# Performance work log

Measured on AMD Instinct MI355X. Metric: run time of the kernel, lower is better.

The kernel has to match this reference:

```python
import jax, jax.numpy as jnp
import numpy as np

H = 2048      # num_hidden
B = 2048      # batch_size
T = 64        # seq_length
C = 10        # num_classes


def setup_inputs() -> dict:
    key = jax.random.key(0)
    k = jax.random.split(key, 4)
    bound = float(np.sqrt(1.0 / H))  # uniform(-bound, bound) init as in the torch module
    return {
        "x": jax.random.normal(k[0], (B, T), dtype=jnp.float32),
        "W_hx": jax.random.uniform(k[1], (H, 1), jnp.float32, -bound, bound),
        "W_hh": jax.random.uniform(k[2], (H, H), jnp.float32, -bound, bound),
        "W_hy": jax.random.uniform(k[3], (H, C), jnp.float32, -bound, bound),
        "b_h": jnp.zeros((H, 1), jnp.float32),
        "b_p": jnp.zeros((C, 1), jnp.float32),
    }


def reference(x, W_hx, W_hh, W_hy, b_h, b_p):
    # x: [B, T]; hidden state kept as [H, B] to match the torch layout.
    xT = x.T  # [T, B] so scan iterates over time

    def step(h, xt):
        # W_hx @ x_t  : [H,1] @ [1,B] -> [H,B]; W_hh @ h : [H,B]
        h = jnp.tanh(W_hx @ xt[None, :] + W_hh @ h + b_h)
        return h, None

    h0 = jnp.zeros((W_hh.shape[0], x.shape[0]), x.dtype)
    hT, _ = jax.lax.scan(step, h0, xT)
    out = W_hy.T @ hT + b_p  # [C, B]
    return out.T             # [B, C]
```

## Files before the change

kernel.cpp:

```cpp
#include <hip/hip_runtime.h>
#include <cstdint>
#include <cstddef>
#include <cmath>

#define H  2048
#define BB 2048
#define TT 64
#define NC 10
#define BK 64

typedef __bf16 bf16;
typedef bf16  bf16x8 __attribute__((ext_vector_type(8)));
typedef bf16  bf16x4 __attribute__((ext_vector_type(4)));
typedef float f32x4  __attribute__((ext_vector_type(4)));

__device__ __forceinline__ void load_lds16(const void* g, void* l) {
    __builtin_amdgcn_global_load_lds(
        (__attribute__((address_space(1))) void*)(void*)g,
        (__attribute__((address_space(3))) void*)l,
        16, 0, 0);
}

__global__ void w_shuffle_kernel(const float* __restrict__ Whh,
                                 bf16* __restrict__ Wshuf) {
    int tid = blockIdx.x * blockDim.x + threadIdx.x;
    int sub = tid >> 6;
    int l   = tid & 63;
    int n16 = sub >> 6;
    int k32 = sub & 63;
    int n = n16 * 16 + (l & 15);
    int k = k32 * 32 + (l >> 4) * 8;
    const float* src = Whh + (size_t)n * H + k;
    bf16x8 o;
#pragma unroll
    for (int j = 0; j < 8; ++j) o[j] = (bf16)src[j];
    *(bf16x8*)(Wshuf + (size_t)tid * 8) = o;
}

__global__ void rnn_init(const float* __restrict__ x,
                         const float* __restrict__ Whx,
                         const float* __restrict__ bh,
                         bf16* __restrict__ S) {
    int b  = blockIdx.x;
    int i0 = threadIdx.x * 8;
    float xv = x[(size_t)b * TT];
    bf16x8 o;
#pragma unroll
    for (int j = 0; j < 8; ++j)
        o[j] = (bf16)tanhf(Whx[i0 + j] * xv + bh[i0 + j]);
    *(bf16x8*)(S + (size_t)b * H + i0) = o;
}

__launch_bounds__(256)
__global__ void rnn_step(const float* __restrict__ x,
                         const float* __restrict__ Whx,
                         const float* __restrict__ bh,
                         const bf16*  __restrict__ Wshuf,
                         const bf16*  __restrict__ Sr,
                         bf16* __restrict__ Sw,
                         int t) {
    __shared__ __align__(16) bf16 As[2][128 * BK];

    const int tid  = threadIdx.x;
    const int w    = tid >> 6;
    const int lane = tid & 63;

    const int xcd = blockIdx.x & 7;
    const int loc = blockIdx.x >> 3;
    const int bm0 = (xcd * 2 + (loc & 1)) * 128;
    const int bn0 = (loc >> 1) * 64;

    const int qm   = (w & 1) * 64;
    const int qn   = (w >> 1) * 32;
    const int lrow = lane & 15;
    const int quad = lane >> 4;

    const int s_r = tid >> 3;
    const int s_l = tid & 7;

    const int nb16 = (bn0 + qn) >> 4;
    const bf16* wb = Wshuf + (size_t)lane * 8;

    auto stageA = [&](int b, int k0) {
#pragma unroll
        for (int i = 0; i < 4; ++i) {
            int r = i * 32 + s_r;
            int g = s_l ^ (r & 7);
            load_lds16(Sr + (size_t)(bm0 + r) * H + k0 + g * 8,
                       &As[b][(i * 256 + w * 64) * 8]);
        }
    };
    auto loadB = [&](bf16x8 (&B)[2][2], int k0) {
        const int kb32 = k0 >> 5;
#pragma unroll
        for (int kc = 0; kc < 2; ++kc)
#pragma unroll
            for (int fn = 0; fn < 2; ++fn)
                B[kc][fn] = *(const bf16x8*)(wb +
                    ((size_t)(nb16 + fn) * 64 + kb32 + kc) * 512);
    };

    f32x4 acc[4][2];
#pragma unroll
    for (int i = 0; i < 4; ++i)
#pragma unroll
        for (int j = 0; j < 2; ++j) acc[i][j] = (f32x4){0.f, 0.f, 0.f, 0.f};

    auto compute = [&](const bf16* Ab, bf16x8 (&B)[2][2]) {
#pragma unroll
        for (int kc = 0; kc < 2; ++kc) {
            bf16x8 af[4];
#pragma unroll
            for (int f = 0; f < 4; ++f) {
                int row = qm + f * 16 + lrow;
                int g   = kc * 4 + quad;
                int l   = g ^ (row & 7);
                af[f] = *(const bf16x8*)&Ab[(row * 8 + l) * 8];
            }
#pragma unroll
            for (int fm = 0; fm < 4; ++fm)
#pragma unroll
                for (int fn = 0; fn < 2; ++fn)
                    acc[fm][fn] = __builtin_amdgcn_mfma_f32_16x16x32_bf16(
                        af[fm], B[kc][fn], acc[fm][fn], 0, 0, 0);
        }
    };

    bf16x8 B0[2][2], B1[2][2];
    stageA(0, 0);
    loadB(B0, 0);

    for (int k0 = 0; k0 < H; k0 += 2 * BK) {
        __syncthreads();
        if (k0 + BK < H) { loadB(B1, k0 + BK); stageA(1, k0 + BK); }
        compute(As[0], B0);

        __syncthreads();
        if (k0 + 2 * BK < H) { loadB(B0, k0 + 2 * BK); stageA(0, k0 + 2 * BK); }
        compute(As[1], B1);
    }

#pragma unroll
    for (int fm = 0; fm < 4; ++fm) {
        int rb = bm0 + qm + fm * 16 + quad * 4;
        float xv[4];
#pragma unroll
        for (int r = 0; r < 4; ++r) xv[r] = x[(size_t)(rb + r) * TT + t];
#pragma unroll
        for (int fn = 0; fn < 2; ++fn) {
            int col = bn0 + qn + fn * 16 + lrow;
            float wx = Whx[col], bb = bh[col];
#pragma unroll
            for (int r = 0; r < 4; ++r) {
                float z = acc[fm][fn][r] + wx * xv[r] + bb;
                Sw[(size_t)(rb + r) * H + col] = (bf16)tanhf(z);
            }
        }
    }
}

__global__ void out_proj(const bf16* __restrict__ S,
                         const float* __restrict__ Why,
                         const float* __restrict__ bp,
                         float* __restrict__ out) {
    int b = blockIdx.x, tid = threadIdx.x;
    float p[NC];
#pragma unroll
    for (int c = 0; c < NC; ++c) p[c] = 0.f;
    for (int h = tid; h < H; h += 256) {
        float s = (float)S[(size_t)b * H + h];
        const float* wr = Why + h * NC;
#pragma unroll
        for (int c = 0; c < NC; ++c) p[c] += s * wr[c];
    }
    __shared__ float red[256 * NC];
#pragma unroll
    for (int c = 0; c < NC; ++c) red[tid * NC + c] = p[c];
    __syncthreads();
    for (int s = 128; s > 0; s >>= 1) {
        if (tid < s)
#pragma unroll
            for (int c = 0; c < NC; ++c) red[tid * NC + c] += red[(tid + s) * NC + c];
        __syncthreads();
    }
    if (tid < NC) out[(size_t)b * NC + tid] = red[tid] + bp[tid];
}

extern "C" void kernel_launch(void* const* d_in, const int* in_sizes, int n_in,
                              void* d_out, int out_size, void* d_ws, size_t ws_size,
                              hipStream_t stream) {
    const float* x   = (const float*)d_in[0];
    const float* Whx = (const float*)d_in[1];
    const float* Whh = (const float*)d_in[2];
    const float* Why = (const float*)d_in[3];
    const float* bh  = (const float*)d_in[4];
    const float* bp  = (const float*)d_in[5];
    float* out = (float*)d_out;

    bf16* Wshuf = (bf16*)d_ws;
    bf16* S0 = (bf16*)((char*)d_ws + (size_t)8 * 1024 * 1024);
    bf16* S1 = (bf16*)((char*)d_ws + (size_t)16 * 1024 * 1024);

    hipLaunchKernelGGL(w_shuffle_kernel, dim3((H * H / 8) / 256), dim3(256),
                       0, stream, Whh, Wshuf);

    hipLaunchKernelGGL(rnn_init, dim3(BB), dim3(256), 0, stream, x, Whx, bh, S1);

    for (int t = 1; t < TT; ++t) {
        const bf16* Srd = (t & 1) ? S1 : S0;
        bf16*       Swr = (t & 1) ? S0 : S1;
        hipLaunchKernelGGL(rnn_step, dim3(512), dim3(256), 0, stream,
                           x, Whx, bh, Wshuf, Srd, Swr, t);
    }

    hipLaunchKernelGGL(out_proj, dim3(BB), dim3(256), 0, stream, S0, Why, bp, out);
}
```

Before: 1.782 ms.

## Drop LDS staging and load A fragments directly from global in 512-thread blocks

The per-step GEMM kernel stops staging the hidden-state tile through shared memory. Each wave now reads its A and B MFMA fragments straight from global memory into registers, double-buffered in registers, with bare s_barrier calls used to keep the waves in step. Blocks grow to 512 threads covering a 128x128 output tile with 256 blocks, so there are fewer, larger blocks. This removes LDS traffic and __syncthreads overhead, but A fragments are no longer shared across waves, so global and L2 traffic goes up and load-latency hiding depends on the register double buffer.

New measurement: 4.792 ms. 169% more time.

```diff
diff --git a/kernel.cpp b/kernel.cpp
--- a/kernel.cpp
+++ b/kernel.cpp
@@ -7,19 +7,10 @@
 #define BB 2048
 #define TT 64
 #define NC 10
-#define BK 64
 
 typedef __bf16 bf16;
 typedef bf16  bf16x8 __attribute__((ext_vector_type(8)));
-typedef bf16  bf16x4 __attribute__((ext_vector_type(4)));
 typedef float f32x4  __attribute__((ext_vector_type(4)));
-
-__device__ __forceinline__ void load_lds16(const void* g, void* l) {
-    __builtin_amdgcn_global_load_lds(
-        (__attribute__((address_space(1))) void*)(void*)g,
-        (__attribute__((address_space(3))) void*)l,
-        16, 0, 0);
-}
 
 __global__ void w_shuffle_kernel(const float* __restrict__ Whh,
                                  bf16* __restrict__ Wshuf) {
@@ -51,7 +42,7 @@
     *(bf16x8*)(S + (size_t)b * H + i0) = o;
 }
 
-__launch_bounds__(256)
+__launch_bounds__(512, 2)
 __global__ void rnn_step(const float* __restrict__ x,
                          const float* __restrict__ Whx,
                          const float* __restrict__ bh,
@@ -59,46 +50,30 @@
                          const bf16*  __restrict__ Sr,
                          bf16* __restrict__ Sw,
                          int t) {
-    __shared__ __align__(16) bf16 As[2][128 * BK];
-
     const int tid  = threadIdx.x;
     const int w    = tid >> 6;
     const int lane = tid & 63;
+    const int lrow = lane & 15;
+    const int quad = lane >> 4;
 
     const int xcd = blockIdx.x & 7;
     const int loc = blockIdx.x >> 3;
     const int bm0 = (xcd * 2 + (loc & 1)) * 128;
-    const int bn0 = (loc >> 1) * 64;
+    const int bn0 = (loc >> 1) * 128;
 
-    const int qm   = (w & 1) * 64;
-    const int qn   = (w >> 1) * 32;
-    const int lrow = lane & 15;
-    const int quad = lane >> 4;
+    const int ms = w & 1;
+    const int ns = w >> 1;
 
-    const int s_r = tid >> 3;
-    const int s_l = tid & 7;
+    const bf16* pA[4];
+#pragma unroll
+    for (int fm = 0; fm < 4; ++fm)
+        pA[fm] = Sr + (size_t)(bm0 + ms * 64 + fm * 16 + lrow) * H + quad * 8;
 
-    const int nb16 = (bn0 + qn) >> 4;
-    const bf16* wb = Wshuf + (size_t)lane * 8;
-
-    auto stageA = [&](int b, int k0) {
+    const bf16* pB[2];
 #pragma unroll
-        for (int i = 0; i < 4; ++i) {
-            int r = i * 32 + s_r;
-            int g = s_l ^ (r & 7);
-            load_lds16(Sr + (size_t)(bm0 + r) * H + k0 + g * 8,
-                       &As[b][(i * 256 + w * 64) * 8]);
-        }
-    };
-    auto loadB = [&](bf16x8 (&B)[2][2], int k0) {
-        const int kb32 = k0 >> 5;
-#pragma unroll
-        for (int kc = 0; kc < 2; ++kc)
-#pragma unroll
-            for (int fn = 0; fn < 2; ++fn)
-                B[kc][fn] = *(const bf16x8*)(wb +
-                    ((size_t)(nb16 + fn) * 64 + kb32 + kc) * 512);
-    };
+    for (int fn = 0; fn < 2; ++fn)
+        pB[fn] = Wshuf + ((size_t)(((bn0 + ns * 32) >> 4) + fn) * 64) * 512
+                       + (size_t)lane * 8;
 
     f32x4 acc[4][2];
 #pragma unroll
@@ -106,49 +81,54 @@
 #pragma unroll
         for (int j = 0; j < 2; ++j) acc[i][j] = (f32x4){0.f, 0.f, 0.f, 0.f};
 
-    auto compute = [&](const bf16* Ab, bf16x8 (&B)[2][2]) {
+    auto loadA = [&](bf16x8 (&Af)[8], int c) {
 #pragma unroll
-        for (int kc = 0; kc < 2; ++kc) {
-            bf16x8 af[4];
+        for (int kc = 0; kc < 2; ++kc)
 #pragma unroll
-            for (int f = 0; f < 4; ++f) {
-                int row = qm + f * 16 + lrow;
-                int g   = kc * 4 + quad;
-                int l   = g ^ (row & 7);
-                af[f] = *(const bf16x8*)&Ab[(row * 8 + l) * 8];
-            }
+            for (int fm = 0; fm < 4; ++fm)
+                Af[kc * 4 + fm] = *(const bf16x8*)(pA[fm] + c * 64 + kc * 32);
+    };
+    auto loadBf = [&](bf16x8 (&Bf)[4], int c) {
+#pragma unroll
+        for (int kc = 0; kc < 2; ++kc)
+#pragma unroll
+            for (int fn = 0; fn < 2; ++fn)
+                Bf[kc * 2 + fn] = *(const bf16x8*)(pB[fn] + (c * 2 + kc) * 512);
+    };
+    auto compute = [&](bf16x8 (&Af)[8], bf16x8 (&Bf)[4]) {
+#pragma unroll
+        for (int kc = 0; kc < 2; ++kc)
 #pragma unroll
             for (int fm = 0; fm < 4; ++fm)
 #pragma unroll
                 for (int fn = 0; fn < 2; ++fn)
                     acc[fm][fn] = __builtin_amdgcn_mfma_f32_16x16x32_bf16(
-                        af[fm], B[kc][fn], acc[fm][fn], 0, 0, 0);
-        }
+                        Af[kc * 4 + fm], Bf[kc * 2 + fn], acc[fm][fn], 0, 0, 0);
     };
 
-    bf16x8 B0[2][2], B1[2][2];
-    stageA(0, 0);
-    loadB(B0, 0);
-
-    for (int k0 = 0; k0 < H; k0 += 2 * BK) {
-        __syncthreads();
-        if (k0 + BK < H) { loadB(B1, k0 + BK); stageA(1, k0 + BK); }
-        compute(As[0], B0);
-
-        __syncthreads();
-        if (k0 + 2 * BK < H) { loadB(B0, k0 + 2 * BK); stageA(0, k0 + 2 * BK); }
-        compute(As[1], B1);
+    bf16x8 A0[8], A1[8], B0f[4], B1f[4];
+    loadA(A0, 0);
+    loadBf(B0f, 0);
+#pragma unroll 1
+    for (int c = 0; c < 32; c += 2) {
+        loadA(A1, c + 1);
+        loadBf(B1f, c + 1);
+        __builtin_amdgcn_s_barrier();
+        compute(A0, B0f);
+        if (c + 2 < 32) { loadA(A0, c + 2); loadBf(B0f, c + 2); }
+        __builtin_amdgcn_s_barrier();
+        compute(A1, B1f);
     }
 
 #pragma unroll
     for (int fm = 0; fm < 4; ++fm) {
-        int rb = bm0 + qm + fm * 16 + quad * 4;
+        int rb = bm0 + ms * 64 + fm * 16 + quad * 4;
         float xv[4];
 #pragma unroll
         for (int r = 0; r < 4; ++r) xv[r] = x[(size_t)(rb + r) * TT + t];
 #pragma unroll
         for (int fn = 0; fn < 2; ++fn) {
-            int col = bn0 + qn + fn * 16 + lrow;
+            int col = bn0 + ns * 32 + fn * 16 + lrow;
             float wx = Whx[col], bb = bh[col];
 #pragma unroll
             for (int r = 0; r < 4; ++r) {
@@ -209,7 +189,7 @@
     for (int t = 1; t < TT; ++t) {
         const bf16* Srd = (t & 1) ? S1 : S0;
         bf16*       Swr = (t & 1) ? S0 : S1;
-        hipLaunchKernelGGL(rnn_step, dim3(512), dim3(256), 0, stream,
+        hipLaunchKernelGGL(rnn_step, dim3(256), dim3(512), 0, stream,
                            x, Whx, bh, Wshuf, Srd, Swr, t);
     }
 
```
